# Kernel optimization log

Hardware: AMD Instinct MI355X
Metric: run time of the kernel (lower is better)

The kernel has to match this reference:

```python
import jax, jax.numpy as jnp
import numpy as np

EPS = 1e-08


def setup_inputs() -> dict:
    key = jax.random.key(0)
    k1, k2, k3 = jax.random.split(key, 3)
    N, IN_DIM, OUT_DIM = 8192, 512, 512
    h = jax.random.normal(k1, (N, IN_DIM), dtype=jnp.float32)
    adj = jax.random.randint(k2, (N, N), 0, 2, dtype=jnp.int32)
    # nn.Linear(in_dim, out_dim, bias=False) weight: [out_dim, in_dim]
    W = jax.random.normal(k3, (OUT_DIM, IN_DIM), dtype=jnp.float32) * (1.0 / np.sqrt(IN_DIM))
    return {"h": h, "adj": adj, "W": W}


def reference(h, adj, W):
    # Wh = h @ W^T  -> [N, out_dim]
    Wh = h @ W.T
    N = Wh.shape[0]
    norms = jnp.linalg.norm(Wh, axis=1, keepdims=True)  # [N, 1]
    # cosine similarity [N, N]
    sim = (Wh @ Wh.T) / (norms * norms.T + EPS)
    mask = (adj > 0) | jnp.eye(N, dtype=bool)
    sim_masked = jnp.where(mask, sim, -jnp.inf)
    alpha = jax.nn.softmax(sim_masked, axis=1)
    return alpha @ Wh
```

## Files before the change

kernel.cpp:

```cpp
#include <hip/hip_runtime.h>
#include <hip/hip_bf16.h>
#include <stdint.h>

#define NN 8192
#define DD 512

typedef unsigned short u16;
typedef unsigned long long u64;
typedef __attribute__((ext_vector_type(8))) short short8;
typedef __attribute__((ext_vector_type(4))) float f32x4;

__device__ __forceinline__ void gld_lds16(const void* g, void* l) {
  __builtin_amdgcn_global_load_lds(
      (const __attribute__((address_space(1))) uint32_t*)(uintptr_t)g,
      (__attribute__((address_space(3))) uint32_t*)(uintptr_t)l,
      16, 0, 0);
}

__device__ __forceinline__ u16 f2bf(float f) {
  __hip_bfloat16 b = __float2bfloat16(f);
  return __builtin_bit_cast(u16, b);
}

__global__ void fill_kernel(float* __restrict__ p, int n, float v) {
  int i = blockIdx.x * 256 + threadIdx.x;
  int stride = gridDim.x * 256;
  for (; i < n; i += stride) p[i] = v;
}

__global__ void cvt4_kernel(const float4* __restrict__ src, ushort4* __restrict__ dst, int n4) {
  int i = blockIdx.x * 256 + threadIdx.x;
  int stride = gridDim.x * 256;
  for (; i < n4; i += stride) {
    float4 v = src[i];
    ushort4 o;
    o.x = f2bf(v.x); o.y = f2bf(v.y); o.z = f2bf(v.z); o.w = f2bf(v.w);
    dst[i] = o;
  }
}

__global__ void pack_adj_kernel(const int* __restrict__ adj, u16* __restrict__ mask,
                                float* __restrict__ den) {
  const int row = blockIdx.x;
  const int t = threadIdx.x;
  if (t == 0) den[row] = 0.0f;
  const uint4* arow = (const uint4*)(adj + (size_t)row * NN);
  #pragma unroll
  for (int iter = 0; iter < 2; iter++) {
    const int c16 = iter * 256 + t;
    unsigned int bits = 0;
    #pragma unroll
    for (int g = 0; g < 4; g++) {
      uint4 v = arow[c16 * 4 + g];
      bits |= (v.x ? 1u : 0u) << (g * 4 + 0);
      bits |= (v.y ? 1u : 0u) << (g * 4 + 1);
      bits |= (v.z ? 1u : 0u) << (g * 4 + 2);
      bits |= (v.w ? 1u : 0u) << (g * 4 + 3);
    }
    mask[(size_t)row * (NN / 16) + c16] = (u16)bits;
  }
}

__global__ void rownorm_kernel(const float* __restrict__ Wh, float* __restrict__ invn) {
  int row = blockIdx.x;
  int l = threadIdx.x;
  const float4* p = (const float4*)(Wh + (size_t)row * DD);
  float4 a = p[l], b = p[l + 64];
  float s = a.x*a.x + a.y*a.y + a.z*a.z + a.w*a.w
          + b.x*b.x + b.y*b.y + b.z*b.z + b.w*b.w;
  #pragma unroll
  for (int off = 32; off; off >>= 1) s += __shfl_down(s, off);
  if (l == 0) invn[row] = 1.0f / sqrtf(s);
}

__global__ void u_wht_kernel(const float* __restrict__ Wh, const float* __restrict__ invn,
                             u16* __restrict__ U, u16* __restrict__ WhT) {
  __shared__ float tile[64][65];
  int i0 = blockIdx.x * 64, d0 = blockIdx.y * 64;
  int c = threadIdx.x & 63, rb = threadIdx.x >> 6;
  #pragma unroll
  for (int r = rb; r < 64; r += 4) {
    float v = Wh[(size_t)(i0 + r) * DD + d0 + c];
    tile[r][c] = v;
    U[(size_t)(i0 + r) * DD + d0 + c] = f2bf(v * invn[i0 + r]);
  }
  __syncthreads();
  #pragma unroll
  for (int r = rb; r < 64; r += 4) {
    WhT[(size_t)(d0 + r) * NN + i0 + c] = f2bf(tile[c][r]);
  }
}

__global__ void __launch_bounds__(256) gemm_wh(
    const u16* __restrict__ A, const u16* __restrict__ B,
    int Nn, int K, float* __restrict__ Cf)
{
  __shared__ __align__(16) u16 As[128 * 32];
  __shared__ __align__(16) u16 Bs[128 * 32];

  const int tid = threadIdx.x;
  const int w = tid >> 6;
  const int lane = tid & 63;
  const int lm = lane & 15;
  const int q = lane >> 4;
  const int row0 = blockIdx.y * 128;
  const int col0 = blockIdx.x * 128;
  const int RM = (w >> 1) * 64;
  const int RN = (w & 1) * 64;
  const int sr = tid >> 2;
  const int sk = (tid & 3) * 8;

  f32x4 acc[4][4];
  #pragma unroll
  for (int a_ = 0; a_ < 4; a_++)
    #pragma unroll
    for (int b_ = 0; b_ < 4; b_++)
      acc[a_][b_] = (f32x4){0.f, 0.f, 0.f, 0.f};

  const size_t Abase = (size_t)row0 * K;
  const size_t Bbase = (size_t)col0 * K;

  for (int k0 = 0; k0 < K; k0 += 32) {
    __syncthreads();
    gld_lds16(A + Abase + (size_t)sr * K + k0 + sk,        (char*)As + w * 1024);
    gld_lds16(A + Abase + (size_t)(sr + 64) * K + k0 + sk, (char*)As + 4096 + w * 1024);
    gld_lds16(B + Bbase + (size_t)sr * K + k0 + sk,        (char*)Bs + w * 1024);
    gld_lds16(B + Bbase + (size_t)(sr + 64) * K + k0 + sk, (char*)Bs + 4096 + w * 1024);
    __syncthreads();

    short8 af[4], bfr[4];
    #pragma unroll
    for (int mt = 0; mt < 4; mt++)
      af[mt] = *(const short8*)&As[(RM + mt * 16 + lm) * 32 + q * 8];
    #pragma unroll
    for (int nt = 0; nt < 4; nt++)
      bfr[nt] = *(const short8*)&Bs[(RN + nt * 16 + lm) * 32 + q * 8];

    #pragma unroll
    for (int mt = 0; mt < 4; mt++)
      #pragma unroll
      for (int nt = 0; nt < 4; nt++)
        acc[mt][nt] = __builtin_amdgcn_mfma_f32_16x16x32_bf16(af[mt], bfr[nt], acc[mt][nt], 0, 0, 0);
  }

  #pragma unroll
  for (int mt = 0; mt < 4; mt++) {
    const int ib = row0 + RM + mt * 16 + q * 4;
    #pragma unroll
    for (int rr = 0; rr < 4; rr++) {
      const int i = ib + rr;
      #pragma unroll
      for (int nt = 0; nt < 4; nt++) {
        const int jc = col0 + RN + nt * 16 + lm;
        Cf[(size_t)i * Nn + jc] = acc[mt][nt][rr];
      }
    }
  }
}

__global__ void __launch_bounds__(256) gemm_sim(
    const u16* __restrict__ U, const u64* __restrict__ maskw,
    u16* __restrict__ Pb, float* __restrict__ den)
{
  __shared__ __align__(16) u16 As[128 * 32];
  __shared__ __align__(16) u16 Bs[128 * 32];

  const int b = blockIdx.x;
  int bi = (int)((sqrtf(8.0f * (float)b + 1.0f) - 1.0f) * 0.5f);
  while ((bi + 1) * (bi + 2) / 2 <= b) bi++;
  while (bi * (bi + 1) / 2 > b) bi--;
  const int bj = b - bi * (bi + 1) / 2;

  const int tid = threadIdx.x;
  const int w = tid >> 6;
  const int lane = tid & 63;
  const int lm = lane & 15;
  const int q = lane >> 4;
  const int row0 = bi * 128;
  const int col0 = bj * 128;
  const int RM = (w >> 1) * 64;
  const int RN = (w & 1) * 64;
  const int sr = tid >> 2;
  const int sk = (tid & 3) * 8;
  const bool diag = (bi == bj);

  f32x4 acc[4][4];
  #pragma unroll
  for (int a_ = 0; a_ < 4; a_++)
    #pragma unroll
    for (int b_ = 0; b_ < 4; b_++)
      acc[a_][b_] = (f32x4){0.f, 0.f, 0.f, 0.f};

  const size_t Abase = (size_t)row0 * DD;
  const size_t Bbase = (size_t)col0 * DD;

  for (int k0 = 0; k0 < DD; k0 += 32) {
    __syncthreads();
    gld_lds16(U + Abase + (size_t)sr * DD + k0 + sk,        (char*)As + w * 1024);
    gld_lds16(U + Abase + (size_t)(sr + 64) * DD + k0 + sk, (char*)As + 4096 + w * 1024);
    gld_lds16(U + Bbase + (size_t)sr * DD + k0 + sk,        (char*)Bs + w * 1024);
    gld_lds16(U + Bbase + (size_t)(sr + 64) * DD + k0 + sk, (char*)Bs + 4096 + w * 1024);
    __syncthreads();

    short8 af[4], bfr[4];
    #pragma unroll
    for (int mt = 0; mt < 4; mt++)
      af[mt] = *(const short8*)&As[(RM + mt * 16 + lm) * 32 + q * 8];
    #pragma unroll
    for (int nt = 0; nt < 4; nt++)
      bfr[nt] = *(const short8*)&Bs[(RN + nt * 16 + lm) * 32 + q * 8];

    #pragma unroll
    for (int mt = 0; mt < 4; mt++)
      #pragma unroll
      for (int nt = 0; nt < 4; nt++)
        acc[mt][nt] = __builtin_amdgcn_mfma_f32_16x16x32_bf16(af[mt], bfr[nt], acc[mt][nt], 0, 0, 0);
  }

  const int wordIdx = (col0 + RN) >> 6;
  const int word2Idx = (row0 + RM) >> 6;

  u64 wrd2[4];
  if (!diag) {
    #pragma unroll
    for (int nt = 0; nt < 4; nt++) {
      const int jc = col0 + RN + nt * 16 + lm;
      wrd2[nt] = maskw[(size_t)jc * (NN / 64) + word2Idx];
    }
  }

  float msum[4] = {0.f, 0.f, 0.f, 0.f};

  #pragma unroll
  for (int mt = 0; mt < 4; mt++) {
    const int ib = row0 + RM + mt * 16 + q * 4;
    float pm[4][4];
    #pragma unroll
    for (int rr = 0; rr < 4; rr++) {
      const int i = ib + rr;
      const u64 wrd = maskw[(size_t)i * (NN / 64) + wordIdx];
      const int bit2 = mt * 16 + q * 4 + rr;
      float psum = 0.f;
      #pragma unroll
      for (int nt = 0; nt < 4; nt++) {
        const int jc = col0 + RN + nt * 16 + lm;
        const float ev = __expf(acc[mt][nt][rr]);
        const bool on = ((wrd >> (nt * 16 + lm)) & 1ull) || (diag && i == jc);
        const float p = on ? ev : 0.0f;
        psum += p;
        Pb[(size_t)i * NN + jc] = f2bf(p);
        if (!diag) {
          const bool on2 = (wrd2[nt] >> bit2) & 1ull;
          const float pmv = on2 ? ev : 0.0f;
          pm[nt][rr] = pmv;
          msum[nt] += pmv;
        }
      }
      #pragma unroll
      for (int off = 8; off; off >>= 1) psum += __shfl_down(psum, off, 16);
      if (lm == 0) atomicAdd(&den[i], psum);
    }
    if (!diag) {
      #pragma unroll
      for (int nt = 0; nt < 4; nt++) {
        const int jc = col0 + RN + nt * 16 + lm;
        ushort4 m4;
        m4.x = f2bf(pm[nt][0]); m4.y = f2bf(pm[nt][1]);
        m4.z = f2bf(pm[nt][2]); m4.w = f2bf(pm[nt][3]);
        *(ushort4*)&Pb[(size_t)jc * NN + ib] = m4;
      }
    }
  }

  if (!diag) {
    #pragma unroll
    for (int nt = 0; nt < 4; nt++) {
      float s = msum[nt];
      s += __shfl_xor(s, 16);
      s += __shfl_xor(s, 32);
      if (q == 0) atomicAdd(&den[col0 + RN + nt * 16 + lm], s);
    }
  }
}

__global__ void __launch_bounds__(512, 2) gemm_out(
    const u16* __restrict__ A,
    const u16* __restrict__ B,
    u16* __restrict__ p0, u16* __restrict__ p1,
    u16* __restrict__ p2, u16* __restrict__ p3)
{
  __shared__ __align__(16) u16 As[128 * 32];
  __shared__ __align__(16) u16 Bs[512 * 32];

  const int tid = threadIdx.x;
  const int w = tid >> 6;
  const int lane = tid & 63;
  const int lm = lane & 15;
  const int q = lane >> 4;
  const int row0 = blockIdx.x * 128;
  const int z = blockIdx.y;
  const int RM = (w >> 2) * 64;
  const int RN = (w & 3) * 128;
  const int sr = tid >> 2;
  const int sk = (tid & 3) * 8;

  f32x4 acc[4][8];
  #pragma unroll
  for (int a_ = 0; a_ < 4; a_++)
    #pragma unroll
    for (int b_ = 0; b_ < 8; b_++)
      acc[a_][b_] = (f32x4){0.f, 0.f, 0.f, 0.f};

  const size_t Abase = (size_t)row0 * NN;
  const int kBegin = z * (NN / 4), kEnd = (z + 1) * (NN / 4);

  for (int k0 = kBegin; k0 < kEnd; k0 += 32) {
    __syncthreads();
    gld_lds16(A + Abase + (size_t)sr * NN + k0 + sk, (char*)As + w * 1024);
    #pragma unroll
    for (int c = 0; c < 4; c++)
      gld_lds16(B + (size_t)(c * 128 + sr) * NN + k0 + sk, (char*)Bs + c * 8192 + w * 1024);
    __syncthreads();

    short8 af[4], bfr[8];
    #pragma unroll
    for (int mt = 0; mt < 4; mt++)
      af[mt] = *(const short8*)&As[(RM + mt * 16 + lm) * 32 + q * 8];
    #pragma unroll
    for (int nt = 0; nt < 8; nt++)
      bfr[nt] = *(const short8*)&Bs[(RN + nt * 16 + lm) * 32 + q * 8];

    #pragma unroll
    for (int mt = 0; mt < 4; mt++)
      #pragma unroll
      for (int nt = 0; nt < 8; nt++)
        acc[mt][nt] = __builtin_amdgcn_mfma_f32_16x16x32_bf16(af[mt], bfr[nt], acc[mt][nt], 0, 0, 0);
  }

  u16* const part = (z == 0) ? p0 : (z == 1) ? p1 : (z == 2) ? p2 : p3;
  #pragma unroll
  for (int mt = 0; mt < 4; mt++) {
    const int ib = row0 + RM + mt * 16 + q * 4;
    #pragma unroll
    for (int rr = 0; rr < 4; rr++) {
      const int i = ib + rr;
      #pragma unroll
      for (int nt = 0; nt < 8; nt++) {
        const int dc = RN + nt * 16 + lm;
        part[(size_t)i * DD + dc] = f2bf(acc[mt][nt][rr]);
      }
    }
  }
}

__global__ void reduce4_kernel(const uint4* __restrict__ p0, const uint4* __restrict__ p1,
                               const uint4* __restrict__ p2, const uint4* __restrict__ p3,
                               const float* __restrict__ den, float4* __restrict__ out) {
  const int idx = blockIdx.x * 256 + threadIdx.x;
  const int row = idx >> 6;
  const float dinv = 1.0f / den[row];
  float s[8] = {0, 0, 0, 0, 0, 0, 0, 0};
  #pragma unroll
  for (int zp = 0; zp < 4; zp++) {
    const uint4 u = (zp == 0 ? p0 : zp == 1 ? p1 : zp == 2 ? p2 : p3)[idx];
    s[0] += __uint_as_float(u.x << 16); s[1] += __uint_as_float(u.x & 0xffff0000u);
    s[2] += __uint_as_float(u.y << 16); s[3] += __uint_as_float(u.y & 0xffff0000u);
    s[4] += __uint_as_float(u.z << 16); s[5] += __uint_as_float(u.z & 0xffff0000u);
    s[6] += __uint_as_float(u.w << 16); s[7] += __uint_as_float(u.w & 0xffff0000u);
  }
  float4 o0 = {s[0] * dinv, s[1] * dinv, s[2] * dinv, s[3] * dinv};
  float4 o1 = {s[4] * dinv, s[5] * dinv, s[6] * dinv, s[7] * dinv};
  out[idx * 2] = o0;
  out[idx * 2 + 1] = o1;
}

extern "C" void kernel_launch(void* const* d_in, const int* in_sizes, int n_in,
                              void* d_out, int out_size, void* d_ws, size_t ws_size,
                              hipStream_t stream) {
  const float* h = (const float*)d_in[0];
  const int* adj = (const int*)d_in[1];
  const float* W = (const float*)d_in[2];
  float* out = (float*)d_out;

  const size_t SZ_P    = (size_t)NN * NN * 2;
  const size_t SZ_MASK = (size_t)NN * NN / 8;
  const size_t SZ_WHT  = (size_t)DD * NN * 2;
  const size_t SZ_HB   = (size_t)NN * DD * 2;
  const size_t SZ_WB   = (size_t)DD * DD * 2;
  const size_t SZ_U    = (size_t)NN * DD * 2;
  const size_t SZ_P3   = (size_t)NN * DD * 2;
  const size_t NEEDED  = SZ_P + SZ_MASK + SZ_WHT + SZ_HB + SZ_WB + SZ_U + SZ_P3 + 2 * (size_t)NN * 4;

  if (ws_size < NEEDED) {
    fill_kernel<<<256, 256, 0, stream>>>(out, out_size, 12345.0f);
    return;
  }

  char* ws = (char*)d_ws;
  size_t off = 0;
  u16*   P    = (u16*)(ws + off); off += SZ_P;
  u16*   mask = (u16*)(ws + off); off += SZ_MASK;
  u16*   WhT  = (u16*)(ws + off); off += SZ_WHT;
  u16*   hb   = (u16*)(ws + off); off += SZ_HB;
  u16*   Wb   = (u16*)(ws + off); off += SZ_WB;
  u16*   U    = (u16*)(ws + off); off += SZ_U;
  u16*   p3   = (u16*)(ws + off); off += SZ_P3;
  float* invn = (float*)(ws + off);
  float* den  = invn + NN;

  float* Wh = (float*)P;
  u16* part0 = mask;
  u16* part1 = U;
  u16* part2 = hb;
  u16* part3 = p3;

  pack_adj_kernel<<<NN, 256, 0, stream>>>(adj, mask, den);
  cvt4_kernel<<<1024, 256, 0, stream>>>((const float4*)h, (ushort4*)hb, NN * DD / 4);
  cvt4_kernel<<<256, 256, 0, stream>>>((const float4*)W, (ushort4*)Wb, DD * DD / 4);
  gemm_wh<<<dim3(DD / 128, NN / 128), 256, 0, stream>>>(hb, Wb, DD, DD, Wh);
  rownorm_kernel<<<NN, 64, 0, stream>>>(Wh, invn);
  u_wht_kernel<<<dim3(NN / 64, DD / 64), 256, 0, stream>>>(Wh, invn, U, WhT);
  gemm_sim<<<64 * 65 / 2, 256, 0, stream>>>(U, (const u64*)mask, P, den);
  gemm_out<<<dim3(NN / 128, 4), 512, 0, stream>>>(P, WhT, part0, part1, part2, part3);
  reduce4_kernel<<<NN * DD / 8 / 256, 256, 0, stream>>>(
      (const uint4*)part0, (const uint4*)part1, (const uint4*)part2, (const uint4*)part3,
      den, (float4*)out);
}
```

Measured before the change: 649.8 us.

## Widen symmetric sim tiles to 128x256 and split output GEMM K eight ways

The symmetric similarity GEMM now uses 128x256 tiles over the lower triangle, with per-element jc<=i masking in place of whole-block diagonal handling. This cuts block count and raises MFMA work per LDS load. The output GEMM splits K into 8 chunks instead of 4 to expose more parallelism, at the cost of more bf16 partial traffic and an 8-way reduce. Workspace aliasing is removed in favour of dedicated Wh and partial buffers, which raises the workspace requirement.

```diff
diff --git a/kernel.cpp b/kernel.cpp
--- a/kernel.cpp
+++ b/kernel.cpp
@@ -163,13 +163,12 @@
     u16* __restrict__ Pb, float* __restrict__ den)
 {
   __shared__ __align__(16) u16 As[128 * 32];
-  __shared__ __align__(16) u16 Bs[128 * 32];
-
-  const int b = blockIdx.x;
-  int bi = (int)((sqrtf(8.0f * (float)b + 1.0f) - 1.0f) * 0.5f);
-  while ((bi + 1) * (bi + 2) / 2 <= b) bi++;
-  while (bi * (bi + 1) / 2 > b) bi--;
-  const int bj = b - bi * (bi + 1) / 2;
+  __shared__ __align__(16) u16 Bs[256 * 32];
+
+  int b = blockIdx.x;
+  int bi = 0, cum = 0;
+  while (cum + ((bi >> 1) + 1) <= b) { cum += (bi >> 1) + 1; bi++; }
+  const int bj2 = b - cum;
 
   const int tid = threadIdx.x;
   const int w = tid >> 6;
@@ -177,117 +176,120 @@
   const int lm = lane & 15;
   const int q = lane >> 4;
   const int row0 = bi * 128;
-  const int col0 = bj * 128;
+  const int col0 = bj2 * 256;
   const int RM = (w >> 1) * 64;
-  const int RN = (w & 1) * 64;
-  const int sr = tid >> 2;
-  const int sk = (tid & 3) * 8;
-  const bool diag = (bi == bj);
-
-  f32x4 acc[4][4];
+  const int RN = (w & 1) * 128;
+
+  f32x4 acc[4][8];
   #pragma unroll
   for (int a_ = 0; a_ < 4; a_++)
     #pragma unroll
-    for (int b_ = 0; b_ < 4; b_++)
+    for (int b_ = 0; b_ < 8; b_++)
       acc[a_][b_] = (f32x4){0.f, 0.f, 0.f, 0.f};
 
   const size_t Abase = (size_t)row0 * DD;
   const size_t Bbase = (size_t)col0 * DD;
+  const int sr4 = tid >> 2;
+  const int sk4 = (tid & 3) * 8;
 
   for (int k0 = 0; k0 < DD; k0 += 32) {
     __syncthreads();
-    gld_lds16(U + Abase + (size_t)sr * DD + k0 + sk,        (char*)As + w * 1024);
-    gld_lds16(U + Abase + (size_t)(sr + 64) * DD + k0 + sk, (char*)As + 4096 + w * 1024);
-    gld_lds16(U + Bbase + (size_t)sr * DD + k0 + sk,        (char*)Bs + w * 1024);
-    gld_lds16(U + Bbase + (size_t)(sr + 64) * DD + k0 + sk, (char*)Bs + 4096 + w * 1024);
-    __syncthreads();
-
-    short8 af[4], bfr[4];
+    #pragma unroll
+    for (int c = 0; c < 2; c++)
+      gld_lds16(U + Abase + (size_t)(c * 64 + sr4) * DD + k0 + sk4,
+                (char*)As + c * 4096 + w * 1024);
+    #pragma unroll
+    for (int c = 0; c < 4; c++)
+      gld_lds16(U + Bbase + (size_t)(c * 64 + sr4) * DD + k0 + sk4,
+                (char*)Bs + c * 4096 + w * 1024);
+    __syncthreads();
+
+    short8 af[4], bfr[8];
     #pragma unroll
     for (int mt = 0; mt < 4; mt++)
       af[mt] = *(const short8*)&As[(RM + mt * 16 + lm) * 32 + q * 8];
     #pragma unroll
-    for (int nt = 0; nt < 4; nt++)
+    for (int nt = 0; nt < 8; nt++)
       bfr[nt] = *(const short8*)&Bs[(RN + nt * 16 + lm) * 32 + q * 8];
 
     #pragma unroll
     for (int mt = 0; mt < 4; mt++)
       #pragma unroll
-      for (int nt = 0; nt < 4; nt++)
+      for (int nt = 0; nt < 8; nt++)
         acc[mt][nt] = __builtin_amdgcn_mfma_f32_16x16x32_bf16(af[mt], bfr[nt], acc[mt][nt], 0, 0, 0);
   }
 
-  const int wordIdx = (col0 + RN) >> 6;
-  const int word2Idx = (row0 + RM) >> 6;
-
-  u64 wrd2[4];
-  if (!diag) {
-    #pragma unroll
-    for (int nt = 0; nt < 4; nt++) {
-      const int jc = col0 + RN + nt * 16 + lm;
-      wrd2[nt] = maskw[(size_t)jc * (NN / 64) + word2Idx];
-    }
-  }
-
-  float msum[4] = {0.f, 0.f, 0.f, 0.f};
+  const int wA = (col0 + RN) >> 6;
+  const int wM = (row0 + RM) >> 6;
+
+  u64 wrd2[8];
+  #pragma unroll
+  for (int nt = 0; nt < 8; nt++) {
+    const int jc = col0 + RN + nt * 16 + lm;
+    wrd2[nt] = maskw[(size_t)jc * (NN / 64) + wM];
+  }
+
+  float msum[8] = {0.f, 0.f, 0.f, 0.f, 0.f, 0.f, 0.f, 0.f};
 
   #pragma unroll
   for (int mt = 0; mt < 4; mt++) {
     const int ib = row0 + RM + mt * 16 + q * 4;
-    float pm[4][4];
+    float pm[8][4];
     #pragma unroll
     for (int rr = 0; rr < 4; rr++) {
       const int i = ib + rr;
-      const u64 wrd = maskw[(size_t)i * (NN / 64) + wordIdx];
+      const u64 nw0 = maskw[(size_t)i * (NN / 64) + wA];
+      const u64 nw1 = maskw[(size_t)i * (NN / 64) + wA + 1];
       const int bit2 = mt * 16 + q * 4 + rr;
       float psum = 0.f;
       #pragma unroll
-      for (int nt = 0; nt < 4; nt++) {
+      for (int nt = 0; nt < 8; nt++) {
         const int jc = col0 + RN + nt * 16 + lm;
         const float ev = __expf(acc[mt][nt][rr]);
-        const bool on = ((wrd >> (nt * 16 + lm)) & 1ull) || (diag && i == jc);
-        const float p = on ? ev : 0.0f;
-        psum += p;
-        Pb[(size_t)i * NN + jc] = f2bf(p);
-        if (!diag) {
-          const bool on2 = (wrd2[nt] >> bit2) & 1ull;
-          const float pmv = on2 ? ev : 0.0f;
-          pm[nt][rr] = pmv;
-          msum[nt] += pmv;
+        const u64 nw = (nt < 4) ? nw0 : nw1;
+        const bool on = ((nw >> ((nt * 16 + lm) & 63)) & 1ull) || (i == jc);
+        if (jc <= i) {
+          const float p = on ? ev : 0.0f;
+          psum += p;
+          Pb[(size_t)i * NN + jc] = f2bf(p);
         }
+        const bool on2 = (wrd2[nt] >> bit2) & 1ull;
+        const float pmv = (jc < i && on2) ? ev : 0.0f;
+        pm[nt][rr] = pmv;
+        msum[nt] += pmv;
       }
       #pragma unroll
       for (int off = 8; off; off >>= 1) psum += __shfl_down(psum, off, 16);
       if (lm == 0) atomicAdd(&den[i], psum);
     }
-    if (!diag) {
-      #pragma unroll
-      for (int nt = 0; nt < 4; nt++) {
-        const int jc = col0 + RN + nt * 16 + lm;
+    #pragma unroll
+    for (int nt = 0; nt < 8; nt++) {
+      const int jc = col0 + RN + nt * 16 + lm;
+      if (jc < ib) {
         ushort4 m4;
         m4.x = f2bf(pm[nt][0]); m4.y = f2bf(pm[nt][1]);
         m4.z = f2bf(pm[nt][2]); m4.w = f2bf(pm[nt][3]);
         *(ushort4*)&Pb[(size_t)jc * NN + ib] = m4;
+      } else if (jc < ib + 4) {
+        for (int rr = jc - ib + 1; rr < 4; rr++)
+          Pb[(size_t)jc * NN + ib + rr] = f2bf(pm[nt][rr]);
       }
     }
   }
 
-  if (!diag) {
-    #pragma unroll
-    for (int nt = 0; nt < 4; nt++) {
-      float s = msum[nt];
-      s += __shfl_xor(s, 16);
-      s += __shfl_xor(s, 32);
-      if (q == 0) atomicAdd(&den[col0 + RN + nt * 16 + lm], s);
-    }
+  #pragma unroll
+  for (int nt = 0; nt < 8; nt++) {
+    float s = msum[nt];
+    s += __shfl_xor(s, 16);
+    s += __shfl_xor(s, 32);
+    if (q == 0) atomicAdd(&den[col0 + RN + nt * 16 + lm], s);
   }
 }
 
 __global__ void __launch_bounds__(512, 2) gemm_out(
     const u16* __restrict__ A,
     const u16* __restrict__ B,
-    u16* __restrict__ p0, u16* __restrict__ p1,
-    u16* __restrict__ p2, u16* __restrict__ p3)
+    u16* __restrict__ part)
 {
   __shared__ __align__(16) u16 As[128 * 32];
   __shared__ __align__(16) u16 Bs[512 * 32];
@@ -312,7 +314,7 @@
       acc[a_][b_] = (f32x4){0.f, 0.f, 0.f, 0.f};
 
   const size_t Abase = (size_t)row0 * NN;
-  const int kBegin = z * (NN / 4), kEnd = (z + 1) * (NN / 4);
+  const int kBegin = z * (NN / 8), kEnd = (z + 1) * (NN / 8);
 
   for (int k0 = kBegin; k0 < kEnd; k0 += 32) {
     __syncthreads();
@@ -337,7 +339,7 @@
         acc[mt][nt] = __builtin_amdgcn_mfma_f32_16x16x32_bf16(af[mt], bfr[nt], acc[mt][nt], 0, 0, 0);
   }
 
-  u16* const part = (z == 0) ? p0 : (z == 1) ? p1 : (z == 2) ? p2 : p3;
+  u16* const pz = part + (size_t)z * NN * DD;
   #pragma unroll
   for (int mt = 0; mt < 4; mt++) {
     const int ib = row0 + RM + mt * 16 + q * 4;
@@ -347,22 +349,21 @@
       #pragma unroll
       for (int nt = 0; nt < 8; nt++) {
         const int dc = RN + nt * 16 + lm;
-        part[(size_t)i * DD + dc] = f2bf(acc[mt][nt][rr]);
+        pz[(size_t)i * DD + dc] = f2bf(acc[mt][nt][rr]);
       }
     }
   }
 }
 
-__global__ void reduce4_kernel(const uint4* __restrict__ p0, const uint4* __restrict__ p1,
-                               const uint4* __restrict__ p2, const uint4* __restrict__ p3,
+__global__ void reduce8_kernel(const u16* __restrict__ part,
                                const float* __restrict__ den, float4* __restrict__ out) {
   const int idx = blockIdx.x * 256 + threadIdx.x;
   const int row = idx >> 6;
   const float dinv = 1.0f / den[row];
   float s[8] = {0, 0, 0, 0, 0, 0, 0, 0};
   #pragma unroll
-  for (int zp = 0; zp < 4; zp++) {
-    const uint4 u = (zp == 0 ? p0 : zp == 1 ? p1 : zp == 2 ? p2 : p3)[idx];
+  for (int zp = 0; zp < 8; zp++) {
+    const uint4 u = ((const uint4*)(part + (size_t)zp * NN * DD))[idx];
     s[0] += __uint_as_float(u.x << 16); s[1] += __uint_as_float(u.x & 0xffff0000u);
     s[2] += __uint_as_float(u.y << 16); s[3] += __uint_as_float(u.y & 0xffff0000u);
     s[4] += __uint_as_float(u.z << 16); s[5] += __uint_as_float(u.z & 0xffff0000u);
@@ -388,8 +389,10 @@
   const size_t SZ_HB   = (size_t)NN * DD * 2;
   const size_t SZ_WB   = (size_t)DD * DD * 2;
   const size_t SZ_U    = (size_t)NN * DD * 2;
-  const size_t SZ_P3   = (size_t)NN * DD * 2;
-  const size_t NEEDED  = SZ_P + SZ_MASK + SZ_WHT + SZ_HB + SZ_WB + SZ_U + SZ_P3 + 2 * (size_t)NN * 4;
+  const size_t SZ_WH   = (size_t)NN * DD * 4;
+  const size_t SZ_PART = (size_t)8 * NN * DD * 2;
+  const size_t NEEDED  = SZ_P + SZ_MASK + SZ_WHT + SZ_HB + SZ_WB + SZ_U + SZ_WH
+                       + SZ_PART + 2 * (size_t)NN * 4;
 
   if (ws_size < NEEDED) {
     fill_kernel<<<256, 256, 0, stream>>>(out, out_size, 12345.0f);
@@ -404,15 +407,10 @@
   u16*   hb   = (u16*)(ws + off); off += SZ_HB;
   u16*   Wb   = (u16*)(ws + off); off += SZ_WB;
   u16*   U    = (u16*)(ws + off); off += SZ_U;
-  u16*   p3   = (u16*)(ws + off); off += SZ_P3;
+  float* Wh   = (float*)(ws + off); off += SZ_WH;
+  u16*   part = (u16*)(ws + off); off += SZ_PART;
   float* invn = (float*)(ws + off);
   float* den  = invn + NN;
-
-  float* Wh = (float*)P;
-  u16* part0 = mask;
-  u16* part1 = U;
-  u16* part2 = hb;
-  u16* part3 = p3;
 
   pack_adj_kernel<<<NN, 256, 0, stream>>>(adj, mask, den);
   cvt4_kernel<<<1024, 256, 0, stream>>>((const float4*)h, (ushort4*)hb, NN * DD / 4);
@@ -420,9 +418,7 @@
   gemm_wh<<<dim3(DD / 128, NN / 128), 256, 0, stream>>>(hb, Wb, DD, DD, Wh);
   rownorm_kernel<<<NN, 64, 0, stream>>>(Wh, invn);
   u_wht_kernel<<<dim3(NN / 64, DD / 64), 256, 0, stream>>>(Wh, invn, U, WhT);
-  gemm_sim<<<64 * 65 / 2, 256, 0, stream>>>(U, (const u64*)mask, P, den);
-  gemm_out<<<dim3(NN / 128, 4), 512, 0, stream>>>(P, WhT, part0, part1, part2, part3);
-  reduce4_kernel<<<NN * DD / 8 / 256, 256, 0, stream>>>(
-      (const uint4*)part0, (const uint4*)part1, (const uint4*)part2, (const uint4*)part3,
-      den, (float4*)out);
-}
+  gemm_sim<<<1056, 256, 0, stream>>>(U, (const u64*)mask, P, den);
+  gemm_out<<<dim3(NN / 128, 8), 512, 0, stream>>>(P, WhT, part);
+  reduce8_kernel<<<NN * DD / 8 / 256, 256, 0, stream>>>(part, den, (float4*)out);
+}
```

After: 720.4 us. 1.11x slower.
